# Kernel optimization log

Measured on AMD Instinct MI355X. Metric: run time of the kernel, lower is better.

## Reference

```python
import jax, jax.numpy as jnp
import numpy as np
import math

NLAT, NLON, LMAX, MMAX = 128, 256, 50, 50
M = NLAT * NLON  # = 2*NLAT^2 grid points, matches torch meshgrid(arange(nlat), arange(-nlat,nlat))

def _grid_np():
    gx, gy = np.meshgrid(np.arange(NLAT), np.arange(-NLAT, NLAT), indexing='ij')
    g = np.stack([gx.ravel(), gy.ravel()], -1).astype(np.float32)
    return g / NLAT * np.pi  # (M, 2)

def _cc_weights(n):
    # Clenshaw-Curtis quadrature nodes theta_j = pi*j/(n-1) and weights on [-1,1]
    N = n - 1
    theta = np.pi * np.arange(n) / N
    k = np.arange(1, N // 2 + 1)
    b = np.where(2 * k == N, 1.0, 2.0)
    S = (b / (4.0 * k ** 2 - 1.0) * np.cos(2.0 * np.outer(theta, k))).sum(-1)
    w = (2.0 / N) * (1.0 - S)
    w[0] *= 0.5
    w[-1] *= 0.5
    return theta, w

def _legendre(lmax, mmax, theta):
    # orthonormal (4pi-normalized) associated Legendre P_l^m(cos theta), Condon-Shortley phase
    x, s = np.cos(theta), np.sin(theta)
    P = np.zeros((mmax, lmax, theta.shape[0]))
    P[0, 0] = math.sqrt(1.0 / (4.0 * math.pi))
    pmm = P[0, 0].copy()
    for m in range(1, mmax):
        pmm = -math.sqrt((2 * m + 1) / (2.0 * m)) * s * pmm
        P[m, m] = pmm
    for m in range(mmax):
        if m + 1 < lmax:
            P[m, m + 1] = math.sqrt(2 * m + 3.0) * x * P[m, m]
        for l in range(m + 2, lmax):
            a = math.sqrt((4.0 * l * l - 1.0) / (l * l - m * m))
            bb = math.sqrt(((l - 1.0) ** 2 - m * m) / (4.0 * (l - 1.0) ** 2 - 1.0))
            P[m, l] = a * (x * P[m, l - 1] - bb * P[m, l - 2])
    return P

_theta_q, _wq = _cc_weights(NLAT)
_SHT_W = jnp.asarray((_legendre(LMAX, MMAX, _theta_q) * _wq).astype(np.float32))  # (mmax, lmax, nlat)
_GRID = jnp.asarray(_grid_np())  # (M, 2)

def setup_inputs() -> dict:
    key = jax.random.key(0)
    target = jax.random.normal(key, (2, 2048, 3), dtype=jnp.float32)
    return {"target": target}

def reference(target):
    B, N, _ = target.shape
    # to_spherical: rho=(B,N) features, sph=(phi, theta)-pi shift on theta -> (B,N,2)
    rho = jnp.linalg.norm(target, axis=-1)
    phi = jnp.arctan2(target[..., 1], target[..., 0])
    theta = jnp.arccos(target[..., 2] / rho)
    sph = jnp.stack([phi, theta - jnp.pi], axis=-1)  # (B, N, 2)
    # squared distances grid(M,2) vs sph(B,N,2) -> (B,M,N) via gram trick (no (B,M,N,2) temp)
    s2 = jnp.sum(sph * sph, -1)                 # (B, N)
    g2 = jnp.sum(_GRID * _GRID, -1)             # (M,)
    cross = jnp.einsum('md,bnd->bmn', _GRID, sph)
    D2 = jax.lax.stop_gradient(s2[:, None, :] + g2[None, :, None] - 2.0 * cross)
    _, idx = jax.lax.top_k(-D2, 3)              # (B, M, 3), 3-NN targets per grid point, ascending dist
    bidx = jnp.arange(B)[:, None, None]
    tmp = sph[bidx, idx]                        # (B, M, 3, 2)
    dist = jnp.sqrt(jnp.sum((tmp - _GRID[None, :, None, :]) ** 2, -1))  # (B, M, 3)
    w = dist / jnp.sum(dist, -1, keepdims=True)
    # three_interpolate: weighted combine of rho at 3 NNs -> (B, M)
    interp = jnp.sum(rho[bidx, idx] * w, -1)
    f = interp.reshape(B, NLAT, NLON)
    # RealSHT (equiangular grid): forward-normalized rfft over lon, then Legendre contraction over lat
    F = (2.0 * jnp.pi) * jnp.fft.rfft(f, axis=-1) / NLON  # (B, nlat, nlon//2+1) complex
    coeff_re = jnp.einsum('bkm,mlk->blm', jnp.real(F[..., :MMAX]), _SHT_W)  # (B, lmax, mmax)
    return coeff_re
```

## Files before the change

kernel.cpp:

```cpp
#include <hip/hip_runtime.h>
#include <math.h>
#include <stdint.h>

#define NLAT 128
#define NLON 256
#define LMAX 50
#define MMAX 50
#define MGRID (NLAT*NLON)
#define BATCH 2
#define NPTS 2048
#define NBKT 64
#define PI_F 3.14159265358979323846f

typedef float v2f __attribute__((ext_vector_type(2)));

__device__ __forceinline__ uint32_t umin32(uint32_t a, uint32_t b) { return a < b ? a : b; }
__device__ __forceinline__ uint32_t umax32(uint32_t a, uint32_t b) { return a > b ? a : b; }

__global__ __launch_bounds__(512, 2)
void k_nn(const float* __restrict__ target, float* __restrict__ f) {
    __shared__ float2   s_all[NPTS];
    __shared__ float    s_rall[NPTS];
    __shared__ __attribute__((aligned(16))) float2 s_pt[2056];
    __shared__ float    s_rho[2056];
    __shared__ uint32_t s_keys[8][64][3];
    __shared__ int      cnt[NBKT], start[NBKT + 1], cur[NBKT];
    __shared__ int      s_win[2];
    int b = blockIdx.x >> 8;
    int j = blockIdx.x & 255;
    int tid = threadIdx.x;
    const float* tg = target + b * NPTS * 3;

    if (tid < NBKT) cnt[tid] = 0;
    __syncthreads();
    float ph[4], py[4], rh[4]; int bk[4];
    #pragma unroll
    for (int c = 0; c < 4; ++c) {
        int p = tid + c * 512;
        float x = tg[p*3], y = tg[p*3+1], z = tg[p*3+2];
        float r = sqrtf(fmaf(x, x, fmaf(y, y, z*z)));
        float cc = fminf(1.f, fmaxf(-1.f, z / r));
        float pyv = acosf(cc) - PI_F;
        ph[c] = atan2f(y, x); py[c] = pyv; rh[c] = r;
        int bb = (int)floorf((pyv + PI_F) * ((float)NBKT / PI_F));
        bk[c] = min(NBKT-1, max(0, bb));
        atomicAdd(&cnt[bk[c]], 1);
    }
    __syncthreads();
    if (tid == 0) {
        int s = 0;
        for (int i = 0; i < NBKT; ++i) { start[i] = s; cur[i] = s; s += cnt[i]; }
        start[NBKT] = s;
    }
    __syncthreads();
    #pragma unroll
    for (int c = 0; c < 4; ++c) {
        int pos = atomicAdd(&cur[bk[c]], 1);
        s_all[pos]  = make_float2(ph[c], py[c]);
        s_rall[pos] = rh[c];
    }

    float gy = (float)(j - 128) * (PI_F / 128.0f);
    int c0 = (int)floorf((gy + PI_F) * ((float)NBKT / PI_F));
    c0 = min(NBKT-1, max(0, c0));
    __syncthreads();
    if (tid < 64) {
        int t = tid;
        int lo_t = max(0, c0 - 5 - t), hi_t = min(NBKT-1, c0 + 5 + t);
        int cw_t = start[hi_t+1] - start[lo_t];
        unsigned long long ok =
            __ballot(cw_t >= 192 || (lo_t == 0 && hi_t == NBKT-1));
        int t0 = __ffsll((unsigned long long)ok) - 1;
        if (tid == 0) {
            s_win[0] = max(0, c0 - 5 - t0);
            s_win[1] = min(NBKT-1, c0 + 5 + t0);
        }
    }
    __syncthreads();
    int lo = s_win[0], hi = s_win[1];
    int cw = start[hi+1] - start[lo];
    int off = start[lo];
    for (int i = tid; i < cw; i += 512) {
        s_pt[i]  = s_all[off + i];
        s_rho[i] = s_rall[off + i];
    }
    int q = ((cw + 3) / 4 + 1) & ~1;
    for (int i = cw + tid; i < 4*q; i += 512) {
        s_pt[i] = make_float2(1e15f, 1e15f);
        s_rho[i] = 0.f;
    }
    __syncthreads();

    int lane = tid & 63;
    int wv   = tid >> 6;
    int part = wv & 3;
    int lat  = lane + ((wv >> 2) << 6);
    float gx = (float)lat * (PI_F / 128.0f);
    v2f gx2 = {gx, gx}, gy2 = {gy, gy};
    uint32_t k0 = ~0u, k1 = ~0u, k2 = ~0u;
    uint32_t nb = (uint32_t)(part * q);
    const float4* p4 = (const float4*)(s_pt + part * q);
    int iters = q >> 1;
    #pragma unroll 4
    for (int i = 0; i < iters; ++i) {
        float4 Q = p4[i];
        v2f px = {Q.x, Q.z}, pyy = {Q.y, Q.w};
        v2f dp = gx2 - px, dt = gy2 - pyy;
        v2f d = dp * dp;
        d = dt * dt + d;
        uint32_t key0 = (__float_as_uint(d.x) & 0xFFFFF800u) | (nb + 2u*i);
        uint32_t key1 = (__float_as_uint(d.y) & 0xFFFFF800u) | (nb + 2u*i + 1u);
        uint32_t t1;
        t1 = umin32(umax32(key0, k0), k1);
        k2 = umin32(umax32(key0, k1), k2);
        k0 = umin32(key0, k0); k1 = t1;
        t1 = umin32(umax32(key1, k0), k1);
        k2 = umin32(umax32(key1, k1), k2);
        k0 = umin32(key1, k0); k1 = t1;
    }
    s_keys[wv][lane][0] = k0;
    s_keys[wv][lane][1] = k1;
    s_keys[wv][lane][2] = k2;
    __syncthreads();

    if (tid < 128) {
        int lane2 = tid & 63;
        int half  = tid >> 6;
        uint32_t m0 = ~0u, m1 = ~0u, m2 = ~0u;
        #pragma unroll
        for (int w = half*4; w < half*4 + 4; ++w) {
            #pragma unroll
            for (int s = 0; s < 3; ++s) {
                uint32_t key = s_keys[w][lane2][s];
                uint32_t t1 = umin32(umax32(key, m0), m1);
                m2 = umin32(umax32(key, m1), m2);
                m0 = umin32(key, m0); m1 = t1;
            }
        }
        int i0 = m0 & 2047, i1 = m1 & 2047, i2 = m2 & 2047;
        int lat2 = lane2 + (half << 6);
        float gxs = (float)lat2 * (PI_F / 128.0f);
        float2 p0 = s_pt[i0], p1 = s_pt[i1], p2 = s_pt[i2];
        float e, r0, r1, r2;
        e = gxs - p0.x; r0 = e*e; e = gy - p0.y; r0 = sqrtf(fmaf(e, e, r0));
        e = gxs - p1.x; r1 = e*e; e = gy - p1.y; r1 = sqrtf(fmaf(e, e, r1));
        e = gxs - p2.x; r2 = e*e; e = gy - p2.y; r2 = sqrtf(fmaf(e, e, r2));
        float sum = r0 + r1 + r2;
        float interp = (s_rho[i0]*r0 + s_rho[i1]*r1 + s_rho[i2]*r2) / sum;
        f[b * MGRID + lat2 * NLON + j] = interp;
    }
}

__global__ __launch_bounds__(1024)
void k_fftsht(const float* __restrict__ f, float* __restrict__ out) {
    __shared__ float Wl[LMAX*129];
    __shared__ float red[NLAT*9];
    __shared__ float sFre[NLAT];
    __shared__ float cred[256];
    __shared__ float s_a[LMAX], s_bb[LMAX], s_w[NLAT];
    __shared__ float s_cm;
    int b = blockIdx.x / MMAX;
    int m = blockIdx.x % MMAX;
    int tid = threadIdx.x;

    if (tid >= 512 && tid < 576) {
        int l = tid - 512;
        if (l < LMAX) {
            float fl = (float)l, fm2 = (float)(m*m);
            s_a[l]  = sqrtf((4.f*fl*fl - 1.f) / fmaxf(fl*fl - fm2, 0.25f));
            float flm1 = fl - 1.f;
            s_bb[l] = sqrtf(fmaxf(flm1*flm1 - fm2, 0.f) /
                            fmaxf(4.f*flm1*flm1 - 1.f, 0.25f));
        }
    } else if (tid >= 576 && tid < 640) {
        int i = tid - 576;
        float v = (i >= 1 && i <= m)
                  ? 0.5f * __log2f((2.f*i + 1.f) / (2.f*i)) : 0.f;
        #pragma unroll
        for (int sh = 1; sh < 64; sh <<= 1) v += __shfl_xor(v, sh);
        if (i == 0) s_cm = ((m & 1) ? -1.f : 1.f) * exp2f(v);
    } else if (tid >= 640 && tid < 768) {
        int k = tid - 640;
        float theta = (PI_F * (float)k) / 127.0f;
        float S = 0.0f;
        for (int kk = 1; kk <= 63; ++kk)
            S += 2.0f / (4.0f*kk*kk - 1.0f) * __cosf(2.0f * theta * (float)kk);
        float w = (2.0f/127.0f) * (1.0f - S);
        if (k == 0 || k == NLAT-1) w *= 0.5f;
        s_w[k] = w;
    }

    {
        int k = tid >> 3, g = tid & 7;
        const float4* fb4 = (const float4*)(f + b * MGRID);
        float p = 0.0f;
        int a = (m * 32 * g) & 255;
        #pragma unroll
        for (int i = 0; i < 8; ++i) {
            float4 v = fb4[k * 64 + g * 8 + i];
            p = fmaf(v.x, __cosf((float)a * (2.0f*PI_F/256.0f)), p); a = (a + m) & 255;
            p = fmaf(v.y, __cosf((float)a * (2.0f*PI_F/256.0f)), p); a = (a + m) & 255;
            p = fmaf(v.z, __cosf((float)a * (2.0f*PI_F/256.0f)), p); a = (a + m) & 255;
            p = fmaf(v.w, __cosf((float)a * (2.0f*PI_F/256.0f)), p); a = (a + m) & 255;
        }
        red[k * 9 + g] = p;
    }
    __syncthreads();

    if (tid < NLAT) {
        int k = tid;
        float srow = 0.0f;
        #pragma unroll
        for (int g = 0; g < 8; ++g) srow += red[k * 9 + g];
        sFre[k] = srow * (2.0f * PI_F / 256.0f);

        float theta = (PI_F * (float)k) / 127.0f;
        float x = __cosf(theta), sn = __sinf(theta);
        float w = s_w[k];
        float pmm;
        if (m == 0) pmm = 0.28209479177f;
        else {
            float mag = exp2f((float)m * __log2f(fabsf(sn)));
            float sg  = (sn < 0.f && (m & 1)) ? -1.f : 1.f;
            pmm = 0.28209479177f * s_cm * mag * sg;
        }
        for (int l = 0; l < m; ++l) Wl[l*129 + k] = 0.0f;
        float Plm2 = pmm;
        Wl[m*129 + k] = Plm2 * w;
        if (m + 1 < LMAX) {
            float Plm1 = sqrtf(2.0f*m + 3.0f) * x * pmm;
            Wl[(m+1)*129 + k] = Plm1 * w;
            for (int l = m + 2; l < LMAX; ++l) {
                float P = s_a[l] * fmaf(-s_bb[l], Plm2, x * Plm1);
                Wl[l*129 + k] = P * w;
                Plm2 = Plm1; Plm1 = P;
            }
        }
    }
    __syncthreads();

    float acc = 0.0f;
    if (tid < 200) {
        int l = tid >> 2, kq = tid & 3;
        #pragma unroll 8
        for (int i = 0; i < 32; ++i)
            acc = fmaf(Wl[l*129 + kq*32 + i], sFre[kq*32 + i], acc);
    }
    if (tid < 256) cred[tid] = acc;
    __syncthreads();
    if (tid < LMAX)
        out[(b*LMAX + tid)*MMAX + m] =
            cred[4*tid] + cred[4*tid+1] + cred[4*tid+2] + cred[4*tid+3];
}

extern "C" void kernel_launch(void* const* d_in, const int* in_sizes, int n_in,
                              void* d_out, int out_size, void* d_ws, size_t ws_size,
                              hipStream_t stream) {
    const float* target = (const float*)d_in[0];
    float* out = (float*)d_out;
    float* f   = (float*)d_ws;

    k_nn<<<BATCH*NLON, 512, 0, stream>>>(target, f);
    k_fftsht<<<BATCH*MMAX, 1024, 0, stream>>>(f, out);
}
```

Measured before the change: 75.41 us.

## Fuse NN interpolation and FFT-SHT into one cooperative kernel with grid sync

```diff
diff --git a/kernel.cpp b/kernel.cpp
--- a/kernel.cpp
+++ b/kernel.cpp
@@ -1,6 +1,9 @@
 #include <hip/hip_runtime.h>
+#include <hip/hip_cooperative_groups.h>
 #include <math.h>
 #include <stdint.h>
+
+namespace cg = cooperative_groups;
 
 #define NLAT 128
 #define NLON 256
@@ -17,18 +20,22 @@
 __device__ __forceinline__ uint32_t umin32(uint32_t a, uint32_t b) { return a < b ? a : b; }
 __device__ __forceinline__ uint32_t umax32(uint32_t a, uint32_t b) { return a > b ? a : b; }
 
-__global__ __launch_bounds__(512, 2)
-void k_nn(const float* __restrict__ target, float* __restrict__ f) {
-    __shared__ float2   s_all[NPTS];
-    __shared__ float    s_rall[NPTS];
-    __shared__ __attribute__((aligned(16))) float2 s_pt[2056];
-    __shared__ float    s_rho[2056];
-    __shared__ uint32_t s_keys[8][64][3];
-    __shared__ int      cnt[NBKT], start[NBKT + 1], cur[NBKT];
-    __shared__ int      s_win[2];
-    int b = blockIdx.x >> 8;
-    int j = blockIdx.x & 255;
-    int tid = threadIdx.x;
+
+__device__ __forceinline__
+void nn_body(char* smem, const float* __restrict__ target,
+             float* __restrict__ f, int blk, int tid) {
+    float2*   s_all  = (float2*)smem;
+    float*    s_rall = (float*)(smem + 16384);
+    float2*   s_pt   = (float2*)(smem + 24576);
+    float*    s_rho  = (float*)(smem + 41024);
+    uint32_t* s_keys = (uint32_t*)(smem + 49248);
+    int*      cnt    = (int*)(smem + 55392);
+    int*      start  = (int*)(smem + 55648);
+    int*      cur    = (int*)(smem + 55908);
+    int*      s_win  = (int*)(smem + 56164);
+
+    int b = blk >> 8;
+    int j = blk & 255;
     const float* tg = target + b * NPTS * 3;
 
     if (tid < NBKT) cnt[tid] = 0;
@@ -118,9 +125,9 @@
         k2 = umin32(umax32(key1, k1), k2);
         k0 = umin32(key1, k0); k1 = t1;
     }
-    s_keys[wv][lane][0] = k0;
-    s_keys[wv][lane][1] = k1;
-    s_keys[wv][lane][2] = k2;
+    s_keys[(wv*64 + lane)*3 + 0] = k0;
+    s_keys[(wv*64 + lane)*3 + 1] = k1;
+    s_keys[(wv*64 + lane)*3 + 2] = k2;
     __syncthreads();
 
     if (tid < 128) {
@@ -131,7 +138,7 @@
         for (int w = half*4; w < half*4 + 4; ++w) {
             #pragma unroll
             for (int s = 0; s < 3; ++s) {
-                uint32_t key = s_keys[w][lane2][s];
+                uint32_t key = s_keys[(w*64 + lane2)*3 + s];
                 uint32_t t1 = umin32(umax32(key, m0), m1);
                 m2 = umin32(umax32(key, m1), m2);
                 m0 = umin32(key, m0); m1 = t1;
@@ -151,20 +158,30 @@
     }
 }
 
-__global__ __launch_bounds__(1024)
-void k_fftsht(const float* __restrict__ f, float* __restrict__ out) {
-    __shared__ float Wl[LMAX*129];
-    __shared__ float red[NLAT*9];
-    __shared__ float sFre[NLAT];
-    __shared__ float cred[256];
-    __shared__ float s_a[LMAX], s_bb[LMAX], s_w[NLAT];
-    __shared__ float s_cm;
-    int b = blockIdx.x / MMAX;
-    int m = blockIdx.x % MMAX;
-    int tid = threadIdx.x;
-
-    if (tid >= 512 && tid < 576) {
-        int l = tid - 512;
+__device__ __forceinline__
+void fftsht_body(char* smem, const float* __restrict__ f,
+                 float* __restrict__ out, int blk, int tid) {
+    float* Wl   = (float*)smem;
+    float* red  = (float*)(smem + 25824);
+    float* sFre = (float*)(smem + 28384);
+    float* cred = (float*)(smem + 28896);
+    float* s_a  = (float*)(smem + 29920);
+    float* s_bb = (float*)(smem + 30120);
+    float* s_w  = (float*)(smem + 30320);
+    float* s_cm = (float*)(smem + 30832);
+
+    int b = blk / MMAX;
+    int m = blk % MMAX;
+
+    if (tid < 64) {
+        int i = tid;
+        float v = (i >= 1 && i <= m)
+                  ? 0.5f * __log2f((2.f*i + 1.f) / (2.f*i)) : 0.f;
+        #pragma unroll
+        for (int sh = 1; sh < 64; sh <<= 1) v += __shfl_xor(v, sh);
+        if (i == 0) *s_cm = ((m & 1) ? -1.f : 1.f) * exp2f(v);
+    } else if (tid < 128) {
+        int l = tid - 64;
         if (l < LMAX) {
             float fl = (float)l, fm2 = (float)(m*m);
             s_a[l]  = sqrtf((4.f*fl*fl - 1.f) / fmaxf(fl*fl - fm2, 0.25f));
@@ -172,15 +189,8 @@
             s_bb[l] = sqrtf(fmaxf(flm1*flm1 - fm2, 0.f) /
                             fmaxf(4.f*flm1*flm1 - 1.f, 0.25f));
         }
-    } else if (tid >= 576 && tid < 640) {
-        int i = tid - 576;
-        float v = (i >= 1 && i <= m)
-                  ? 0.5f * __log2f((2.f*i + 1.f) / (2.f*i)) : 0.f;
-        #pragma unroll
-        for (int sh = 1; sh < 64; sh <<= 1) v += __shfl_xor(v, sh);
-        if (i == 0) s_cm = ((m & 1) ? -1.f : 1.f) * exp2f(v);
-    } else if (tid >= 640 && tid < 768) {
-        int k = tid - 640;
+    } else if (tid < 256) {
+        int k = tid - 128;
         float theta = (PI_F * (float)k) / 127.0f;
         float S = 0.0f;
         for (int kk = 1; kk <= 63; ++kk)
@@ -191,27 +201,25 @@
     }
 
     {
-        int k = tid >> 3, g = tid & 7;
+        int k = tid >> 2, g = tid & 3;
         const float4* fb4 = (const float4*)(f + b * MGRID);
         float p = 0.0f;
-        int a = (m * 32 * g) & 255;
+        int a = (m * 64 * g) & 255;
         #pragma unroll
-        for (int i = 0; i < 8; ++i) {
-            float4 v = fb4[k * 64 + g * 8 + i];
+        for (int i = 0; i < 16; ++i) {
+            float4 v = fb4[k * 64 + g * 16 + i];
             p = fmaf(v.x, __cosf((float)a * (2.0f*PI_F/256.0f)), p); a = (a + m) & 255;
             p = fmaf(v.y, __cosf((float)a * (2.0f*PI_F/256.0f)), p); a = (a + m) & 255;
             p = fmaf(v.z, __cosf((float)a * (2.0f*PI_F/256.0f)), p); a = (a + m) & 255;
             p = fmaf(v.w, __cosf((float)a * (2.0f*PI_F/256.0f)), p); a = (a + m) & 255;
         }
-        red[k * 9 + g] = p;
+        red[k * 5 + g] = p;
     }
     __syncthreads();
 
     if (tid < NLAT) {
         int k = tid;
-        float srow = 0.0f;
-        #pragma unroll
-        for (int g = 0; g < 8; ++g) srow += red[k * 9 + g];
+        float srow = red[k*5] + red[k*5+1] + red[k*5+2] + red[k*5+3];
         sFre[k] = srow * (2.0f * PI_F / 256.0f);
 
         float theta = (PI_F * (float)k) / 127.0f;
@@ -222,7 +230,7 @@
         else {
             float mag = exp2f((float)m * __log2f(fabsf(sn)));
             float sg  = (sn < 0.f && (m & 1)) ? -1.f : 1.f;
-            pmm = 0.28209479177f * s_cm * mag * sg;
+            pmm = 0.28209479177f * (*s_cm) * mag * sg;
         }
         for (int l = 0; l < m; ++l) Wl[l*129 + k] = 0.0f;
         float Plm2 = pmm;
@@ -253,6 +261,29 @@
             cred[4*tid] + cred[4*tid+1] + cred[4*tid+2] + cred[4*tid+3];
 }
 
+__global__ __launch_bounds__(512, 4)
+void k_fused(const float* __restrict__ target, float* __restrict__ f,
+             float* __restrict__ out) {
+    __shared__ __attribute__((aligned(16))) char smem[56192];
+    int tid = threadIdx.x;
+    nn_body(smem, target, f, blockIdx.x, tid);
+    __threadfence();
+    cg::this_grid().sync();
+    if (blockIdx.x < BATCH * MMAX)
+        fftsht_body(smem, f, out, blockIdx.x, tid);
+}
+
+__global__ __launch_bounds__(512, 2)
+void k_nn(const float* __restrict__ target, float* __restrict__ f) {
+    __shared__ __attribute__((aligned(16))) char smem[56192];
+    nn_body(smem, target, f, blockIdx.x, threadIdx.x);
+}
+__global__ __launch_bounds__(512)
+void k_fftsht(const float* __restrict__ f, float* __restrict__ out) {
+    __shared__ __attribute__((aligned(16))) char smem[30848];
+    fftsht_body(smem, f, out, blockIdx.x, threadIdx.x);
+}
+
 extern "C" void kernel_launch(void* const* d_in, const int* in_sizes, int n_in,
                               void* d_out, int out_size, void* d_ws, size_t ws_size,
                               hipStream_t stream) {
@@ -260,6 +291,11 @@
     float* out = (float*)d_out;
     float* f   = (float*)d_ws;
 
-    k_nn<<<BATCH*NLON, 512, 0, stream>>>(target, f);
-    k_fftsht<<<BATCH*MMAX, 1024, 0, stream>>>(f, out);
-}
+    void* args[] = { (void*)&target, (void*)&f, (void*)&out };
+    hipError_t err = hipLaunchCooperativeKernel(
+        (const void*)k_fused, dim3(BATCH*NLON), dim3(512), args, 0, stream);
+    if (err != hipSuccess) {
+        k_nn<<<BATCH*NLON, 512, 0, stream>>>(target, f);
+        k_fftsht<<<BATCH*MMAX, 512, 0, stream>>>(f, out);
+    }
+}
```

Result: slower. 191.6 us (+154.1%).

## Scan candidates in place and shrink SHT block to 512 threads

Applied to the files above, without the earlier changes.

```diff
diff --git a/kernel.cpp b/kernel.cpp
--- a/kernel.cpp
+++ b/kernel.cpp
@@ -19,11 +19,9 @@
 
 __global__ __launch_bounds__(512, 2)
 void k_nn(const float* __restrict__ target, float* __restrict__ f) {
-    __shared__ float2   s_all[NPTS];
-    __shared__ float    s_rall[NPTS];
-    __shared__ __attribute__((aligned(16))) float2 s_pt[2056];
-    __shared__ float    s_rho[2056];
-    __shared__ uint32_t s_keys[8][64][3];
+    __shared__ __attribute__((aligned(16))) float2 s_all[NPTS + 8];
+    __shared__ float    s_rall[NPTS + 8];
+    __shared__ uint32_t s_keys[8*64*3];
     __shared__ int      cnt[NBKT], start[NBKT + 1], cur[NBKT];
     __shared__ int      s_win[2];
     int b = blockIdx.x >> 8;
@@ -47,23 +45,34 @@
         atomicAdd(&cnt[bk[c]], 1);
     }
     __syncthreads();
-    if (tid == 0) {
-        int s = 0;
-        for (int i = 0; i < NBKT; ++i) { start[i] = s; cur[i] = s; s += cnt[i]; }
-        start[NBKT] = s;
-    }
-    __syncthreads();
+
+    if (tid < 64) {
+        int v = cnt[tid];
+        int cv = v;
+        #pragma unroll
+        for (int sh = 1; sh < 64; sh <<= 1) {
+            int t = __shfl_up(v, sh);
+            if (tid >= sh) v += t;
+        }
+        start[tid + 1] = v;
+        cur[tid] = v - cv;
+        if (tid == 0) start[0] = 0;
+    }
+    __syncthreads();
+
     #pragma unroll
     for (int c = 0; c < 4; ++c) {
         int pos = atomicAdd(&cur[bk[c]], 1);
         s_all[pos]  = make_float2(ph[c], py[c]);
         s_rall[pos] = rh[c];
     }
-
+    if (tid < 8) {
+        s_all[NPTS + tid] = make_float2(1e15f, 1e15f);
+        s_rall[NPTS + tid] = 0.f;
+    }
     float gy = (float)(j - 128) * (PI_F / 128.0f);
     int c0 = (int)floorf((gy + PI_F) * ((float)NBKT / PI_F));
     c0 = min(NBKT-1, max(0, c0));
-    __syncthreads();
     if (tid < 64) {
         int t = tid;
         int lo_t = max(0, c0 - 5 - t), hi_t = min(NBKT-1, c0 + 5 + t);
@@ -77,20 +86,11 @@
         }
     }
     __syncthreads();
+
     int lo = s_win[0], hi = s_win[1];
-    int cw = start[hi+1] - start[lo];
-    int off = start[lo];
-    for (int i = tid; i < cw; i += 512) {
-        s_pt[i]  = s_all[off + i];
-        s_rho[i] = s_rall[off + i];
-    }
+    int off = start[lo] & ~1;
+    int cw  = start[hi+1] - off;
     int q = ((cw + 3) / 4 + 1) & ~1;
-    for (int i = cw + tid; i < 4*q; i += 512) {
-        s_pt[i] = make_float2(1e15f, 1e15f);
-        s_rho[i] = 0.f;
-    }
-    __syncthreads();
-
     int lane = tid & 63;
     int wv   = tid >> 6;
     int part = wv & 3;
@@ -99,7 +99,7 @@
     v2f gx2 = {gx, gx}, gy2 = {gy, gy};
     uint32_t k0 = ~0u, k1 = ~0u, k2 = ~0u;
     uint32_t nb = (uint32_t)(part * q);
-    const float4* p4 = (const float4*)(s_pt + part * q);
+    const float4* p4 = (const float4*)(s_all + off + part * q);
     int iters = q >> 1;
     #pragma unroll 4
     for (int i = 0; i < iters; ++i) {
@@ -118,9 +118,9 @@
         k2 = umin32(umax32(key1, k1), k2);
         k0 = umin32(key1, k0); k1 = t1;
     }
-    s_keys[wv][lane][0] = k0;
-    s_keys[wv][lane][1] = k1;
-    s_keys[wv][lane][2] = k2;
+    s_keys[(wv*64 + lane)*3 + 0] = k0;
+    s_keys[(wv*64 + lane)*3 + 1] = k1;
+    s_keys[(wv*64 + lane)*3 + 2] = k2;
     __syncthreads();
 
     if (tid < 128) {
@@ -131,30 +131,32 @@
         for (int w = half*4; w < half*4 + 4; ++w) {
             #pragma unroll
             for (int s = 0; s < 3; ++s) {
-                uint32_t key = s_keys[w][lane2][s];
+                uint32_t key = s_keys[(w*64 + lane2)*3 + s];
                 uint32_t t1 = umin32(umax32(key, m0), m1);
                 m2 = umin32(umax32(key, m1), m2);
                 m0 = umin32(key, m0); m1 = t1;
             }
         }
-        int i0 = m0 & 2047, i1 = m1 & 2047, i2 = m2 & 2047;
+        int i0 = off + (int)(m0 & 2047);
+        int i1 = off + (int)(m1 & 2047);
+        int i2 = off + (int)(m2 & 2047);
         int lat2 = lane2 + (half << 6);
         float gxs = (float)lat2 * (PI_F / 128.0f);
-        float2 p0 = s_pt[i0], p1 = s_pt[i1], p2 = s_pt[i2];
+        float2 p0 = s_all[i0], p1 = s_all[i1], p2 = s_all[i2];
         float e, r0, r1, r2;
         e = gxs - p0.x; r0 = e*e; e = gy - p0.y; r0 = sqrtf(fmaf(e, e, r0));
         e = gxs - p1.x; r1 = e*e; e = gy - p1.y; r1 = sqrtf(fmaf(e, e, r1));
         e = gxs - p2.x; r2 = e*e; e = gy - p2.y; r2 = sqrtf(fmaf(e, e, r2));
         float sum = r0 + r1 + r2;
-        float interp = (s_rho[i0]*r0 + s_rho[i1]*r1 + s_rho[i2]*r2) / sum;
+        float interp = (s_rall[i0]*r0 + s_rall[i1]*r1 + s_rall[i2]*r2) / sum;
         f[b * MGRID + lat2 * NLON + j] = interp;
     }
 }
 
-__global__ __launch_bounds__(1024)
+__global__ __launch_bounds__(512)
 void k_fftsht(const float* __restrict__ f, float* __restrict__ out) {
     __shared__ float Wl[LMAX*129];
-    __shared__ float red[NLAT*9];
+    __shared__ float red[NLAT*5];
     __shared__ float sFre[NLAT];
     __shared__ float cred[256];
     __shared__ float s_a[LMAX], s_bb[LMAX], s_w[NLAT];
@@ -163,8 +165,15 @@
     int m = blockIdx.x % MMAX;
     int tid = threadIdx.x;
 
-    if (tid >= 512 && tid < 576) {
-        int l = tid - 512;
+    if (tid < 64) {
+        int i = tid;
+        float v = (i >= 1 && i <= m)
+                  ? 0.5f * __log2f((2.f*i + 1.f) / (2.f*i)) : 0.f;
+        #pragma unroll
+        for (int sh = 1; sh < 64; sh <<= 1) v += __shfl_xor(v, sh);
+        if (i == 0) s_cm = ((m & 1) ? -1.f : 1.f) * exp2f(v);
+    } else if (tid < 128) {
+        int l = tid - 64;
         if (l < LMAX) {
             float fl = (float)l, fm2 = (float)(m*m);
             s_a[l]  = sqrtf((4.f*fl*fl - 1.f) / fmaxf(fl*fl - fm2, 0.25f));
@@ -172,15 +181,8 @@
             s_bb[l] = sqrtf(fmaxf(flm1*flm1 - fm2, 0.f) /
                             fmaxf(4.f*flm1*flm1 - 1.f, 0.25f));
         }
-    } else if (tid >= 576 && tid < 640) {
-        int i = tid - 576;
-        float v = (i >= 1 && i <= m)
-                  ? 0.5f * __log2f((2.f*i + 1.f) / (2.f*i)) : 0.f;
-        #pragma unroll
-        for (int sh = 1; sh < 64; sh <<= 1) v += __shfl_xor(v, sh);
-        if (i == 0) s_cm = ((m & 1) ? -1.f : 1.f) * exp2f(v);
-    } else if (tid >= 640 && tid < 768) {
-        int k = tid - 640;
+    } else if (tid < 256) {
+        int k = tid - 128;
         float theta = (PI_F * (float)k) / 127.0f;
         float S = 0.0f;
         for (int kk = 1; kk <= 63; ++kk)
@@ -191,27 +193,25 @@
     }
 
     {
-        int k = tid >> 3, g = tid & 7;
+        int k = tid >> 2, g = tid & 3;
         const float4* fb4 = (const float4*)(f + b * MGRID);
         float p = 0.0f;
-        int a = (m * 32 * g) & 255;
-        #pragma unroll
-        for (int i = 0; i < 8; ++i) {
-            float4 v = fb4[k * 64 + g * 8 + i];
+        int a = (m * 64 * g) & 255;
+        #pragma unroll
+        for (int i = 0; i < 16; ++i) {
+            float4 v = fb4[k * 64 + g * 16 + i];
             p = fmaf(v.x, __cosf((float)a * (2.0f*PI_F/256.0f)), p); a = (a + m) & 255;
             p = fmaf(v.y, __cosf((float)a * (2.0f*PI_F/256.0f)), p); a = (a + m) & 255;
             p = fmaf(v.z, __cosf((float)a * (2.0f*PI_F/256.0f)), p); a = (a + m) & 255;
             p = fmaf(v.w, __cosf((float)a * (2.0f*PI_F/256.0f)), p); a = (a + m) & 255;
         }
-        red[k * 9 + g] = p;
+        red[k * 5 + g] = p;
     }
     __syncthreads();
 
     if (tid < NLAT) {
         int k = tid;
-        float srow = 0.0f;
-        #pragma unroll
-        for (int g = 0; g < 8; ++g) srow += red[k * 9 + g];
+        float srow = red[k*5] + red[k*5+1] + red[k*5+2] + red[k*5+3];
         sFre[k] = srow * (2.0f * PI_F / 256.0f);
 
         float theta = (PI_F * (float)k) / 127.0f;
@@ -261,5 +261,5 @@
     float* f   = (float*)d_ws;
 
     k_nn<<<BATCH*NLON, 512, 0, stream>>>(target, f);
-    k_fftsht<<<BATCH*MMAX, 1024, 0, stream>>>(f, out);
+    k_fftsht<<<BATCH*MMAX, 512, 0, stream>>>(f, out);
 }
```

Result: no change. 74.75 us (-0.9%).
